# Kernel optimization log

Hardware: AMD Instinct MI355X
Metric: run time of the kernel (lower is better)

## Reference

```python
import jax, jax.numpy as jnp
import numpy as np

B, C, QK, T, S = 16, 256, 32, 15, 31


def _conv1x1(x, w, b):
    # 1x1 conv as channel matmul; w: [out, in]
    return jnp.einsum("oc,bchw->bohw", w, x) + b[None, :, None, None]


def _spatial_attn(x, qw, qb, kw, kb, vw, vb, g):
    Bn, Cn, H, W = x.shape
    N = H * W
    q = _conv1x1(x, qw, qb).reshape(Bn, -1, N)  # [B,QK,N]
    k = _conv1x1(x, kw, kb).reshape(Bn, -1, N)  # [B,QK,N]
    v = _conv1x1(x, vw, vb).reshape(Bn, Cn, N)  # [B,C,N]
    energy = jnp.einsum("bqn,bqm->bnm", q, k)   # [B,N,N]
    A = jax.nn.softmax(energy, axis=-1)
    out = g * jnp.einsum("bcm,bnm->bcn", v, A)
    return out.reshape(Bn, Cn, H, W)


def _channel_attn_calc(x):
    Bn, Cn = x.shape[0], x.shape[1]
    f = x.reshape(Bn, Cn, -1)
    e = jnp.einsum("bcn,bdn->bcd", f, f)  # [B,C,C]
    e = jnp.max(e, axis=-1, keepdims=True) - e
    return jax.nn.softmax(e, axis=-1)


def _channel_attn_use(x, A, w):
    Bn, Cn = x.shape[0], x.shape[1]
    v = x.reshape(Bn, Cn, -1)
    return (w * jnp.einsum("bcd,bdn->bcn", A, v)).reshape(x.shape)


def _mod_deform_conv(x, ow, ob, w, b):
    # Modulated deformable conv (DCNv2) 3x3, pad 1, stride 1.
    Bn, Cn, H, W = x.shape
    om = jax.lax.conv_general_dilated(x, ow, (1, 1), ((1, 1), (1, 1)),
                                      dimension_numbers=("NCHW", "OIHW", "NCHW"))
    om = om + ob[None, :, None, None]  # [B,27,H,W]
    off_y, off_x, mask = om[:, :9], om[:, 9:18], jax.nn.sigmoid(om[:, 18:])
    ky, kx = jnp.meshgrid(jnp.arange(3), jnp.arange(3), indexing="ij")
    py = off_y + jnp.arange(H)[None, None, :, None] + (ky.reshape(9) - 1)[None, :, None, None]
    px = off_x + jnp.arange(W)[None, None, None, :] + (kx.reshape(9) - 1)[None, :, None, None]
    y0f = jnp.floor(py); x0f = jnp.floor(px)
    wy = py - y0f; wx = px - x0f
    y0 = y0f.astype(jnp.int32); x0 = x0f.astype(jnp.int32)
    xf = x.reshape(Bn, Cn, H * W)

    def gather(yi, xi, wgt):
        valid = (yi >= 0) & (yi < H) & (xi >= 0) & (xi < W)
        idx = (jnp.clip(yi, 0, H - 1) * W + jnp.clip(xi, 0, W - 1)).reshape(Bn, -1)
        g = jax.vmap(lambda a, i: a[:, i])(xf, idx).reshape(Bn, Cn, 9, H, W)
        return g * (wgt * valid.astype(x.dtype))[:, None]

    val = (gather(y0, x0, (1 - wy) * (1 - wx)) + gather(y0, x0 + 1, (1 - wy) * wx)
           + gather(y0 + 1, x0, wy * (1 - wx)) + gather(y0 + 1, x0 + 1, wy * wx))
    val = val * mask[:, None]  # [B,C,9,H,W]
    return jnp.einsum("bckhw,ock->bohw", val, w.reshape(w.shape[0], Cn, 9)) + b[None, :, None, None]


def _forward(template_features, sr_features,
             t_sp_qw, t_sp_qb, t_sp_kw, t_sp_kb, t_sp_vw, t_sp_vb, t_sp_g,
             s_sp_qw, s_sp_qb, s_sp_kw, s_sp_kb, s_sp_vw, s_sp_vb, s_sp_g,
             w_t_ch, w_s_ch, w_s2t, w_t2s,
             t_off_w, t_off_b, t_dcn_w, t_dcn_b,
             s_off_w, s_off_b, s_dcn_w, s_dcn_b):
    t, s = template_features, sr_features
    t_sp = _spatial_attn(t, t_sp_qw, t_sp_qb, t_sp_kw, t_sp_kb, t_sp_vw, t_sp_vb, t_sp_g)
    s_sp = _spatial_attn(s, s_sp_qw, s_sp_qb, s_sp_kw, s_sp_kb, s_sp_vw, s_sp_vb, s_sp_g)
    tA = _channel_attn_calc(t)
    sA = _channel_attn_calc(s)
    t_ch = _channel_attn_use(t, tA, w_t_ch)
    s_ch = _channel_attn_use(s, sA, w_s_ch)
    t_x = _channel_attn_use(t, sA, w_s2t)   # sr->template cross attention
    s_x = _channel_attn_use(s, tA, w_t2s)   # template->sr cross attention
    t_out = t + t_sp + t_ch + t_x
    s_out = s + s_sp + s_ch + s_x
    t_out = _mod_deform_conv(t_out, t_off_w, t_off_b, t_dcn_w, t_dcn_b)
    s_out = _mod_deform_conv(s_out, s_off_w, s_off_b, s_dcn_w, s_dcn_b)
    return t_out, s_out


def setup_inputs() -> dict:
    key = jax.random.key(0)
    ks = jax.random.split(key, 28)
    r = lambda i, shape, sc=0.05: jax.random.normal(ks[i], shape, dtype=jnp.float32) * sc
    return {
        "template_features": jax.random.normal(ks[0], (B, C, T, T), dtype=jnp.float32),
        "sr_features": jax.random.normal(ks[1], (B, C, S, S), dtype=jnp.float32),
        "t_sp_qw": r(2, (QK, C)), "t_sp_qb": r(3, (QK,)),
        "t_sp_kw": r(4, (QK, C)), "t_sp_kb": r(5, (QK,)),
        "t_sp_vw": r(6, (C, C)), "t_sp_vb": r(7, (C,)), "t_sp_g": r(8, (1,), 0.5),
        "s_sp_qw": r(9, (QK, C)), "s_sp_qb": r(10, (QK,)),
        "s_sp_kw": r(11, (QK, C)), "s_sp_kb": r(12, (QK,)),
        "s_sp_vw": r(13, (C, C)), "s_sp_vb": r(14, (C,)), "s_sp_g": r(15, (1,), 0.5),
        "w_t_ch": r(16, (1,), 0.5), "w_s_ch": r(17, (1,), 0.5),
        "w_s2t": r(18, (1,), 0.5), "w_t2s": r(19, (1,), 0.5),
        "t_off_w": r(20, (27, C, 3, 3), 0.01), "t_off_b": r(21, (27,), 0.01),
        "t_dcn_w": r(22, (C, C, 3, 3)), "t_dcn_b": r(23, (C,)),
        "s_off_w": r(24, (27, C, 3, 3), 0.01), "s_off_b": r(25, (27,), 0.01),
        "s_dcn_w": r(26, (C, C, 3, 3)), "s_dcn_b": r(27, (C,)),
    }


def reference(template_features, sr_features,
              t_sp_qw, t_sp_qb, t_sp_kw, t_sp_kb, t_sp_vw, t_sp_vb, t_sp_g,
              s_sp_qw, s_sp_qb, s_sp_kw, s_sp_kb, s_sp_vw, s_sp_vb, s_sp_g,
              w_t_ch, w_s_ch, w_s2t, w_t2s,
              t_off_w, t_off_b, t_dcn_w, t_dcn_b,
              s_off_w, s_off_b, s_dcn_w, s_dcn_b):
    return _forward(template_features, sr_features,
                    t_sp_qw, t_sp_qb, t_sp_kw, t_sp_kb, t_sp_vw, t_sp_vb, t_sp_g,
                    s_sp_qw, s_sp_qb, s_sp_kw, s_sp_kb, s_sp_vw, s_sp_vb, s_sp_g,
                    w_t_ch, w_s_ch, w_s2t, w_t2s,
                    t_off_w, t_off_b, t_dcn_w, t_dcn_b,
                    s_off_w, s_off_b, s_dcn_w, s_dcn_b)
```

## Files before the change

kernel.cpp:

```cpp
#include <hip/hip_runtime.h>
#include <hip/hip_bf16.h>
#include <cmath>

typedef __attribute__((ext_vector_type(8))) short bf16x8;
typedef __attribute__((ext_vector_type(4))) float f32x4;

__device__ inline ushort f2bf(float f) {
  __hip_bfloat16 h = __float2bfloat16(f);
  return *reinterpret_cast<ushort*>(&h);
}
__device__ inline float bf2f(ushort u) {
  return __uint_as_float((uint)u << 16);
}
__device__ inline float bflo(uint x) { return __uint_as_float(x << 16); }
__device__ inline float bfhi(uint x) { return __uint_as_float(x & 0xffff0000u); }

__device__ inline bool fdecode(int totalS, int gxS, int gyS, int gxT, int gyT,
                               int& bx, int& by, int& bz, bool& isT) {
  const int total = gridDim.x;
  const int id = blockIdx.x;
  int wid = (id & 7) * (total >> 3) + (id >> 3);
  const int totalT = gxT * gyT * 16;
  if (wid >= totalS + totalT) return false;
  isT = wid >= totalS;
  int lid = isT ? wid - totalS : wid;
  const int gx = isT ? gxT : gxS;
  const int gy = isT ? gyT : gyS;
  bx = lid % gx;
  lid /= gx;
  by = lid % gy;
  bz = lid / gy;
  return true;
}

__global__ __launch_bounds__(256) void prep_weights_kernel(
    const float* __restrict__ t_qw, const float* __restrict__ t_qb,
    const float* __restrict__ t_kw, const float* __restrict__ t_kb,
    const float* __restrict__ s_qw, const float* __restrict__ s_qb,
    const float* __restrict__ s_kw, const float* __restrict__ s_kb,
    const float* __restrict__ t_vw, const float* __restrict__ t_vb,
    const float* __restrict__ s_vw, const float* __restrict__ s_vb,
    const float* __restrict__ t_off_w, const float* __restrict__ s_off_w,
    const float* __restrict__ t_dcn_w, const float* __restrict__ s_dcn_w,
    ushort* __restrict__ Wall_t, ushort* __restrict__ Wall_s,
    float* __restrict__ biasAll_t, float* __restrict__ biasAll_s,
    ushort* __restrict__ owb_t, ushort* __restrict__ owb_s,
    ushort* __restrict__ Awb_t, ushort* __restrict__ Awb_s) {
  int i = blockIdx.x * 256 + threadIdx.x;
  if (i < 81920) {
    const int r = i >> 8, c = i & 255;
    float v;
    if (r < 256) v = t_vw[(size_t)r * 256 + c];
    else if (r < 288) v = t_qw[(size_t)(r - 256) * 256 + c];
    else v = t_kw[(size_t)(r - 288) * 256 + c];
    Wall_t[i] = f2bf(v);
    return;
  }
  i -= 81920;
  if (i < 81920) {
    const int r = i >> 8, c = i & 255;
    float v;
    if (r < 256) v = s_vw[(size_t)r * 256 + c];
    else if (r < 288) v = s_qw[(size_t)(r - 256) * 256 + c];
    else v = s_kw[(size_t)(r - 288) * 256 + c];
    Wall_s[i] = f2bf(v);
    return;
  }
  i -= 81920;
  if (i < 320) {
    biasAll_t[i] = (i < 256) ? t_vb[i] : ((i < 288) ? t_qb[i - 256] : t_kb[i - 288]);
    return;
  }
  i -= 320;
  if (i < 320) {
    biasAll_s[i] = (i < 256) ? s_vb[i] : ((i < 288) ? s_qb[i - 256] : s_kb[i - 288]);
    return;
  }
  i -= 320;
  if (i < 73728) {
    const int o = i / 2304, k = i % 2304, tap = k >> 8, c = k & 255;
    owb_t[i] = (o < 27) ? f2bf(t_off_w[(size_t)o * 2304 + c * 9 + tap]) : (ushort)0;
    return;
  }
  i -= 73728;
  if (i < 73728) {
    const int o = i / 2304, k = i % 2304, tap = k >> 8, c = k & 255;
    owb_s[i] = (o < 27) ? f2bf(s_off_w[(size_t)o * 2304 + c * 9 + tap]) : (ushort)0;
    return;
  }
  i -= 73728;
  if (i < 589824) {
    const int frag = i >> 9, within = i & 511;
    const int lane = within >> 3, j = within & 7;
    const int mt = frag / 72, kt = frag % 72;
    const int o = mt * 16 + (lane & 15);
    const int k = kt * 32 + (lane >> 4) * 8 + j;
    const int tap = k >> 8, c = k & 255;
    Awb_t[i] = f2bf(t_dcn_w[(size_t)o * 2304 + c * 9 + tap]);
    return;
  }
  i -= 589824;
  if (i < 589824) {
    const int frag = i >> 9, within = i & 511;
    const int lane = within >> 3, j = within & 7;
    const int mt = frag / 72, kt = frag % 72;
    const int o = mt * 16 + (lane & 15);
    const int k = kt * 32 + (lane >> 4) * 8 + j;
    const int tap = k >> 8, c = k & 255;
    Awb_s[i] = f2bf(s_dcn_w[(size_t)o * 2304 + c * 9 + tap]);
  }
}

__global__ __launch_bounds__(256) void cast_transpose_fused_kernel(
    const float* __restrict__ xS, ushort* __restrict__ oS, ushort* __restrict__ pS,
    int NS_, int NRS_, int NpS_,
    const float* __restrict__ xT, ushort* __restrict__ oT, ushort* __restrict__ pT,
    int NT_, int NRT_, int NpT_) {
  constexpr int C = 256;
  __shared__ float T[64][65];
  int bx, by, bz; bool isT;
  if (!fdecode(1024, 16, 4, 4, 4, bx, by, bz, isT)) return;
  const float* x = isT ? xT : xS;
  ushort* xTo = isT ? oT : oS;
  ushort* xbf = isT ? pT : pS;
  const int N = isT ? NT_ : NS_;
  const int NR = isT ? NRT_ : NRS_;
  const int Np = isT ? NpT_ : NpS_;
  const int b = bz;
  const int n0 = bx * 64, c0 = by * 64;
  const float* xb = x + (size_t)b * C * N;
  const int tid = threadIdx.x;
  for (int u = tid; u < 4096; u += 256) {
    const int cc = u >> 6, nn = u & 63;
    const int gn = n0 + nn;
    T[cc][nn] = (gn < N) ? xb[(size_t)(c0 + cc) * N + gn] : 0.f;
  }
  __syncthreads();
  ushort* ob = xTo + (size_t)b * NR * C;
  for (int u = tid; u < 4096; u += 256) {
    const int nn = u >> 6, cc = u & 63;
    ob[(size_t)(n0 + nn) * C + c0 + cc] = f2bf(T[cc][nn]);
  }
  ushort* pb = xbf + (size_t)b * C * Np;
  for (int u = tid; u < 4096; u += 256) {
    const int cc = u >> 6, nn = u & 63;
    const int gn = n0 + nn;
    if (gn < Np) pb[(size_t)(c0 + cc) * Np + gn] = f2bf(T[cc][nn]);
  }
}

__global__ __launch_bounds__(256) void proj_fused_kernel(
    const ushort* __restrict__ WallS, const float* __restrict__ bS,
    const ushort* __restrict__ BtS, ushort* __restrict__ vS,
    float* __restrict__ qkS, int NS_, int NpS_, int NRS_,
    const ushort* __restrict__ WallT, const float* __restrict__ bT,
    const ushort* __restrict__ BtT, ushort* __restrict__ vT,
    float* __restrict__ qkT, int NT_, int NpT_, int NRT_) {
  constexpr int C = 256;
  __shared__ ushort Asm[64][40];
  __shared__ ushort Bsm[64][40];
  int bx, by, bz; bool isT;
  if (!fdecode(1280, 16, 5, 4, 5, bx, by, bz, isT)) return;
  const ushort* Wall = isT ? WallT : WallS;
  const float* bias = isT ? bT : bS;
  const ushort* Bt = isT ? BtT : BtS;
  ushort* vbf = isT ? vT : vS;
  float* qk = isT ? qkT : qkS;
  const int N = isT ? NT_ : NS_, Np = isT ? NpT_ : NpS_, NR = isT ? NRT_ : NRS_;
  const int n0 = bx * 64, m0 = by * 64, b = bz;
  const ushort* Ab = Wall + (size_t)m0 * C;
  const ushort* Bb = Bt + (size_t)b * NR * C;
  const int tid = threadIdx.x, lane = tid & 63, w = tid >> 6;
  f32x4 acc[4];
#pragma unroll
  for (int i = 0; i < 4; i++) acc[i] = (f32x4){0.f, 0.f, 0.f, 0.f};
  for (int k0 = 0; k0 < C; k0 += 32) {
    {
      const int row = tid >> 2, seg = tid & 3;
      *reinterpret_cast<uint4*>(&Asm[row][seg * 8]) =
          *reinterpret_cast<const uint4*>(&Ab[(size_t)row * C + k0 + seg * 8]);
    }
    {
      const int row = tid >> 2, seg = tid & 3;
      *reinterpret_cast<uint4*>(&Bsm[row][seg * 8]) =
          *reinterpret_cast<const uint4*>(&Bb[(size_t)(n0 + row) * C + k0 + seg * 8]);
    }
    __syncthreads();
    const int koff = (lane >> 4) * 8;
    const bf16x8 bfr = *reinterpret_cast<const bf16x8*>(&Bsm[w * 16 + (lane & 15)][koff]);
#pragma unroll
    for (int mf = 0; mf < 4; mf++) {
      const bf16x8 af = *reinterpret_cast<const bf16x8*>(&Asm[mf * 16 + (lane & 15)][koff]);
      acc[mf] = __builtin_amdgcn_mfma_f32_16x16x32_bf16(af, bfr, acc[mf], 0, 0, 0);
    }
    __syncthreads();
  }
  const int gn = n0 + w * 16 + (lane & 15);
#pragma unroll
  for (int mf = 0; mf < 4; mf++) {
    const int mbase = m0 + mf * 16 + ((lane >> 4) * 4);
#pragma unroll
    for (int rr = 0; rr < 4; rr++) {
      const int m = mbase + rr;
      if (m < 256) {
        if (gn < Np) {
          ushort v = (gn < N) ? f2bf(acc[mf][rr] + bias[m]) : (ushort)0;
          vbf[((size_t)b * 256 + m) * Np + gn] = v;
        }
      } else {
        if (gn < N)
          qk[((size_t)b * 64 + (m - 256)) * N + gn] = acc[mf][rr] + bias[m];
      }
    }
  }
}

__global__ __launch_bounds__(256) void softmax_mcomb_kernel(
    const float* __restrict__ Atc, const float* __restrict__ Asc,
    const float* __restrict__ w_t_ch, const float* __restrict__ w_s2t,
    const float* __restrict__ w_s_ch, const float* __restrict__ w_t2s,
    ushort* __restrict__ Mc_t, ushort* __restrict__ Mc_s) {
  const int row = blockIdx.x;
  const int tid = threadIdx.x;
  __shared__ float red[8];
  const size_t idx = (size_t)row * 256 + tid;
  const float a = -Atc[idx];
  const float s = -Asc[idx];
  float ma = a, ms = s;
#pragma unroll
  for (int off = 32; off; off >>= 1) {
    ma = fmaxf(ma, __shfl_xor(ma, off, 64));
    ms = fmaxf(ms, __shfl_xor(ms, off, 64));
  }
  if ((tid & 63) == 0) { red[tid >> 6] = ma; red[4 + (tid >> 6)] = ms; }
  __syncthreads();
  if (tid == 0) {
    float m1 = red[0], m2 = red[4];
    for (int i = 1; i < 4; i++) { m1 = fmaxf(m1, red[i]); m2 = fmaxf(m2, red[4 + i]); }
    red[0] = m1; red[4] = m2;
  }
  __syncthreads();
  ma = red[0]; ms = red[4];
  __syncthreads();
  const float ea = __expf(a - ma), es = __expf(s - ms);
  float sa = ea, ss = es;
#pragma unroll
  for (int off = 32; off; off >>= 1) {
    sa += __shfl_xor(sa, off, 64);
    ss += __shfl_xor(ss, off, 64);
  }
  if ((tid & 63) == 0) { red[tid >> 6] = sa; red[4 + (tid >> 6)] = ss; }
  __syncthreads();
  if (tid == 0) {
    float t1 = 0.f, t2 = 0.f;
    for (int i = 0; i < 4; i++) { t1 += red[i]; t2 += red[4 + i]; }
    red[0] = t1; red[4] = t2;
  }
  __syncthreads();
  const float Pa = ea / red[0], Ps = es / red[4];
  Mc_t[idx] = f2bf(w_t_ch[0] * Pa + w_s2t[0] * Ps);
  Mc_s[idx] = f2bf(w_s_ch[0] * Ps + w_t2s[0] * Pa);
}

template <int EPI>
__global__ __launch_bounds__(256) void gemm_fused_kernel(
    const ushort* __restrict__ AS, int aPerB_S, const ushort* __restrict__ BtS,
    const float* __restrict__ biasS, ushort* __restrict__ outBfS,
    float* __restrict__ outFS, int NS_, int NpS_, int NRS_, int KpS_,
    const ushort* __restrict__ AT, int aPerB_T, const ushort* __restrict__ BtT,
    const float* __restrict__ biasT, ushort* __restrict__ outBfT,
    float* __restrict__ outFT, int NT_, int NpT_, int NRT_, int KpT_,
    int totalS, int gxS, int gxT) {
  constexpr int CM = 256, BM = 128, NW = 4, NF = 2, WN = 2;
  __shared__ ushort Asm[BM][40];
  __shared__ ushort Bsm[64][40];
  int bx, by, bz; bool isT;
  if (!fdecode(totalS, gxS, 2, gxT, 2, bx, by, bz, isT)) return;
  const ushort* A = isT ? AT : AS;
  const ushort* Bt = isT ? BtT : BtS;
  const float* bias = isT ? biasT : biasS;
  ushort* outBf = isT ? outBfT : outBfS;
  float* outF = isT ? outFT : outFS;
  const int aPerBatch = isT ? aPerB_T : aPerB_S;
  const int N = isT ? NT_ : NS_, Np = isT ? NpT_ : NpS_;
  const int NR = isT ? NRT_ : NRS_, Kp = isT ? KpT_ : KpS_;
  const int n0 = bx * 64, m0 = by * BM, b = bz;
  const ushort* Ab = A + (size_t)(aPerBatch ? b : 0) * CM * Kp;
  const ushort* Bb = Bt + (size_t)b * NR * Kp;
  const int tid = threadIdx.x, lane = tid & 63, w = tid >> 6;
  const int wr = w / WN, wc = w % WN;
  f32x4 acc[4][NF];
#pragma unroll
  for (int i = 0; i < 4; i++)
#pragma unroll
    for (int j = 0; j < NF; j++) acc[i][j] = (f32x4){0.f, 0.f, 0.f, 0.f};
  for (int k0 = 0; k0 < Kp; k0 += 32) {
    for (int u = tid; u < BM * 4; u += NW * 64) {
      const int row = u >> 2, seg = u & 3;
      *reinterpret_cast<uint4*>(&Asm[row][seg * 8]) =
          *reinterpret_cast<const uint4*>(&Ab[(size_t)(m0 + row) * Kp + k0 + seg * 8]);
    }
    for (int u = tid; u < 64 * 4; u += NW * 64) {
      const int row = u >> 2, seg = u & 3;
      *reinterpret_cast<uint4*>(&Bsm[row][seg * 8]) =
          *reinterpret_cast<const uint4*>(&Bb[(size_t)(n0 + row) * Kp + k0 + seg * 8]);
    }
    __syncthreads();
    const int koff = (lane >> 4) * 8;
    bf16x8 af[4], bfr[NF];
#pragma unroll
    for (int mf = 0; mf < 4; mf++)
      af[mf] = *reinterpret_cast<const bf16x8*>(&Asm[wr * 64 + mf * 16 + (lane & 15)][koff]);
#pragma unroll
    for (int nf = 0; nf < NF; nf++)
      bfr[nf] = *reinterpret_cast<const bf16x8*>(&Bsm[wc * NF * 16 + nf * 16 + (lane & 15)][koff]);
#pragma unroll
    for (int mf = 0; mf < 4; mf++)
#pragma unroll
      for (int nf = 0; nf < NF; nf++)
        acc[mf][nf] = __builtin_amdgcn_mfma_f32_16x16x32_bf16(af[mf], bfr[nf], acc[mf][nf], 0, 0, 0);
    __syncthreads();
  }
#pragma unroll
  for (int mf = 0; mf < 4; mf++) {
    const int mbase = m0 + wr * 64 + mf * 16 + ((lane >> 4) * 4);
#pragma unroll
    for (int nf = 0; nf < NF; nf++) {
      const int gn = n0 + wc * NF * 16 + nf * 16 + (lane & 15);
      if (EPI == 0) {
#pragma unroll
        for (int rr = 0; rr < 4; rr++) {
          const int m = mbase + rr;
          if (gn < Np) {
            ushort v = (gn < N) ? f2bf(acc[mf][nf][rr] + bias[m]) : (ushort)0;
            outBf[((size_t)b * CM + m) * Np + gn] = v;
          }
        }
      } else {
#pragma unroll
        for (int rr = 0; rr < 4; rr++) {
          if (gn < N)
            outF[((size_t)b * CM + mbase + rr) * N + gn] = acc[mf][nf][rr];
        }
      }
    }
  }
  (void)NR;
}

__global__ __launch_bounds__(256) void energy_fused_kernel(
    const float* __restrict__ qkS, ushort* __restrict__ SS, int NS_, int NpS_,
    const float* __restrict__ qkT, ushort* __restrict__ ST, int NT_, int NpT_) {
  __shared__ ushort Aq[64][40];
  __shared__ ushort Bk[64][40];
  int bx, by, bz; bool isT;
  if (!fdecode(4096, 16, 16, 4, 4, bx, by, bz, isT)) return;
  const float* qk = isT ? qkT : qkS;
  ushort* Sbf = isT ? ST : SS;
  const int N = isT ? NT_ : NS_, Np = isT ? NpT_ : NpS_;
  const int m0 = bx * 64, n0 = by * 64, b = bz;
  const float* qb = qk + (size_t)b * 64 * N;
  const float* kb = qb + (size_t)32 * N;
  const int tid = threadIdx.x, lane = tid & 63, w = tid >> 6;
  for (int u = tid; u < 2048; u += 256) {
    const int c = u >> 6, nn = u & 63;
    const int gn = n0 + nn, gm = m0 + nn;
    Aq[nn][c] = (gn < N) ? f2bf(qb[(size_t)c * N + gn]) : (ushort)0;
    Bk[nn][c] = (gm < N) ? f2bf(kb[(size_t)c * N + gm]) : (ushort)0;
  }
  __syncthreads();
  const int koff = (lane >> 4) * 8;
  const bf16x8 af = *reinterpret_cast<const bf16x8*>(&Aq[w * 16 + (lane & 15)][koff]);
  f32x4 acc[4];
#pragma unroll
  for (int j = 0; j < 4; j++) {
    const bf16x8 bf = *reinterpret_cast<const bf16x8*>(&Bk[j * 16 + (lane & 15)][koff]);
    acc[j] = __builtin_amdgcn_mfma_f32_16x16x32_bf16(af, bf, (f32x4){0.f, 0.f, 0.f, 0.f}, 0, 0, 0);
  }
#pragma unroll
  for (int j = 0; j < 4; j++) {
    const int m = m0 + j * 16 + (lane & 15);
    if (m >= Np) continue;
#pragma unroll
    for (int r = 0; r < 4; r++) {
      const int n = n0 + w * 16 + (lane >> 4) * 4 + r;
      if (n < N) Sbf[((size_t)b * N + n) * Np + m] = (m < N) ? f2bf(acc[j][r]) : (ushort)0;
    }
  }
}

__global__ __launch_bounds__(256) void softmax_bf16_fused_kernel(
    ushort* __restrict__ Ss, int Ns, int Nps, ushort* __restrict__ St, int Nt,
    int Npt, int rowsS) {
  __shared__ float buf[992];
  __shared__ float red[4];
  const int row = blockIdx.x;
  ushort* r;
  int N;
  if (row < rowsS) {
    r = Ss + (size_t)row * Nps;
    N = Ns;
  } else {
    r = St + (size_t)(row - rowsS) * Npt;
    N = Nt;
  }
  const int tid = threadIdx.x;
  float mx = -1e30f;
  for (int i = tid; i < N; i += 256) {
    float f = bf2f(r[i]);
    buf[i] = f;
    mx = fmaxf(mx, f);
  }
#pragma unroll
  for (int off = 32; off; off >>= 1) mx = fmaxf(mx, __shfl_xor(mx, off, 64));
  if ((tid & 63) == 0) red[tid >> 6] = mx;
  __syncthreads();
  if (tid == 0) {
    float m2 = red[0];
    for (int i = 1; i < 4; i++) m2 = fmaxf(m2, red[i]);
    red[0] = m2;
  }
  __syncthreads();
  mx = red[0];
  __syncthreads();
  float s = 0.f;
  for (int i = tid; i < N; i += 256) {
    float v = __expf(buf[i] - mx);
    buf[i] = v;
    s += v;
  }
#pragma unroll
  for (int off = 32; off; off >>= 1) s += __shfl_xor(s, off, 64);
  if ((tid & 63) == 0) red[tid >> 6] = s;
  __syncthreads();
  if (tid == 0) {
    float t = 0.f;
    for (int i = 0; i < 4; i++) t += red[i];
    red[0] = t;
  }
  __syncthreads();
  const float inv = 1.f / red[0];
  for (int i = tid; i < N; i += 256) r[i] = f2bf(buf[i] * inv);
}

__global__ __launch_bounds__(256) void pv_chan_fused_kernel(
    const ushort* __restrict__ vS, const ushort* __restrict__ SS,
    const ushort* __restrict__ McS, const ushort* __restrict__ xTS,
    const float* __restrict__ xS, const float* __restrict__ gS,
    ushort* __restrict__ xsTS, int NS_, int NpS_, int NRS_,
    const ushort* __restrict__ vT, const ushort* __restrict__ ST,
    const ushort* __restrict__ McT, const ushort* __restrict__ xTT,
    const float* __restrict__ xT_, const float* __restrict__ gT,
    ushort* __restrict__ xsTT, int NT_, int NpT_, int NRT_) {
  constexpr int C = 256, BM = 128, NW = 4, NF = 2, WN = 2;
  __shared__ ushort Asm[BM][40];
  __shared__ ushort Bsm[64][40];
  int bx, by, bz; bool isT;
  if (!fdecode(512, 16, 2, 4, 2, bx, by, bz, isT)) return;
  const ushort* vbf = isT ? vT : vS;
  const ushort* Sbf = isT ? ST : SS;
  const ushort* Mc = isT ? McT : McS;
  const ushort* xTb = isT ? xTT : xTS;
  const float* x = isT ? xT_ : xS;
  const float* gp = isT ? gT : gS;
  ushort* xsT = isT ? xsTT : xsTS;
  const int N = isT ? NT_ : NS_, Np = isT ? NpT_ : NpS_;
  const int NR = isT ? NRT_ : NRS_;
  const int n0 = bx * 64, m0 = by * BM, b = bz;
  const int tid = threadIdx.x, lane = tid & 63, w = tid >> 6;
  const int wr = w / WN, wc = w % WN;
// ... 330 lines not shown
#pragma unroll
      for (int rr = 0; rr < 4; rr++)
        out[((size_t)b * C + mbase + rr) * N + gn] = acc[mf][rr] + bias[mbase + rr];
    }
  }
}

extern "C" void kernel_launch(void* const* d_in, const int* in_sizes, int n_in,
                              void* d_out, int out_size, void* d_ws, size_t ws_size,
                              hipStream_t stream) {
  const float* t_in = (const float*)d_in[0];
  const float* s_in = (const float*)d_in[1];
  const float* t_qw = (const float*)d_in[2];
  const float* t_qb = (const float*)d_in[3];
  const float* t_kw = (const float*)d_in[4];
  const float* t_kb = (const float*)d_in[5];
  const float* t_vw = (const float*)d_in[6];
  const float* t_vb = (const float*)d_in[7];
  const float* t_g = (const float*)d_in[8];
  const float* s_qw = (const float*)d_in[9];
  const float* s_qb = (const float*)d_in[10];
  const float* s_kw = (const float*)d_in[11];
  const float* s_kb = (const float*)d_in[12];
  const float* s_vw = (const float*)d_in[13];
  const float* s_vb = (const float*)d_in[14];
  const float* s_g = (const float*)d_in[15];
  const float* w_t_ch = (const float*)d_in[16];
  const float* w_s_ch = (const float*)d_in[17];
  const float* w_s2t = (const float*)d_in[18];
  const float* w_t2s = (const float*)d_in[19];
  const float* t_off_w = (const float*)d_in[20];
  const float* t_off_b = (const float*)d_in[21];
  const float* t_dcn_w = (const float*)d_in[22];
  const float* t_dcn_b = (const float*)d_in[23];
  const float* s_off_w = (const float*)d_in[24];
  const float* s_off_b = (const float*)d_in[25];
  const float* s_dcn_w = (const float*)d_in[26];
  const float* s_dcn_b = (const float*)d_in[27];
  (void)in_sizes; (void)n_in; (void)out_size; (void)ws_size;

  constexpr int Bn = 16, C = 256;
  constexpr int HT = 15, WT = 15, NT = HT * WT;
  constexpr int HS = 31, WS2 = 31, NS = HS * WS2;
  constexpr int NpT = 256, NpS = 992;
  constexpr int NRT = 256, NRS = 1024;

  float* ws = (float*)d_ws;
  size_t off = 0;
  auto alloc = [&](size_t n) {
    n = (n + 3) & ~(size_t)3;
    float* p = ws + off; off += n; return p;
  };
  auto allocU = [&](size_t nu) { return (ushort*)alloc((nu + 1) / 2); };

  float* qk_t = alloc((size_t)Bn * 64 * NT);
  float* qk_s = alloc((size_t)Bn * 64 * NS);
  ushort* Wall_t = allocU((size_t)320 * C);
  ushort* Wall_s = allocU((size_t)320 * C);
  float* biasAll_t = alloc(320);
  float* biasAll_s = alloc(320);
  ushort* xT_t = allocU((size_t)Bn * NRT * C);
  ushort* xT_s = allocU((size_t)Bn * NRS * C);
  ushort* xbf_t = allocU((size_t)Bn * C * NpT);
  ushort* xbf_s = allocU((size_t)Bn * C * NpS);
  ushort* v_tbf = allocU((size_t)Bn * C * NpT);
  ushort* v_sbf = allocU((size_t)Bn * C * NpS);
  ushort* S_t = allocU((size_t)Bn * NT * NpT);
  ushort* S_s = allocU((size_t)Bn * NS * NpS);
  ushort* xsT_t = allocU((size_t)Bn * NRT * C);
  ushort* xsT_s = allocU((size_t)Bn * NRS * C);
  float* Atc = alloc((size_t)Bn * C * C);
  float* Asc = alloc((size_t)Bn * C * C);
  ushort* Mc_t = allocU((size_t)Bn * C * C);
  ushort* Mc_s = allocU((size_t)Bn * C * C);
  ushort* owb_t = allocU((size_t)32 * 2304);
  ushort* owb_s = allocU((size_t)32 * 2304);
  ushort* Awb_t = allocU((size_t)256 * 2304);
  ushort* Awb_s = allocU((size_t)256 * 2304);
  uint4* prep_t = (uint4*)alloc((size_t)Bn * 9 * NT * 4);
  uint4* prep_s = (uint4*)alloc((size_t)Bn * 9 * NS * 4);

  dim3 blk(256);

  prep_weights_kernel<<<dim3((1491584 + 255) / 256), blk, 0, stream>>>(
      t_qw, t_qb, t_kw, t_kb, s_qw, s_qb, s_kw, s_kb,
      t_vw, t_vb, s_vw, s_vb, t_off_w, s_off_w, t_dcn_w, s_dcn_w,
      Wall_t, Wall_s, biasAll_t, biasAll_s, owb_t, owb_s, Awb_t, Awb_s);

  cast_transpose_fused_kernel<<<dim3(1280), blk, 0, stream>>>(
      s_in, xT_s, xbf_s, NS, NRS, NpS, t_in, xT_t, xbf_t, NT, NRT, NpT);

  proj_fused_kernel<<<dim3(1600), blk, 0, stream>>>(
      Wall_s, biasAll_s, xT_s, v_sbf, qk_s, NS, NpS, NRS,
      Wall_t, biasAll_t, xT_t, v_tbf, qk_t, NT, NpT, NRT);

  energy_fused_kernel<<<dim3(4352), blk, 0, stream>>>(
      qk_s, S_s, NS, NpS, qk_t, S_t, NT, NpT);

  softmax_bf16_fused_kernel<<<dim3(Bn * NS + Bn * NT), blk, 0, stream>>>(
      S_s, NS, NpS, S_t, NT, NpT, Bn * NS);

  gemm_fused_kernel<2><<<dim3(256), blk, 0, stream>>>(
      xbf_s, 1, xbf_s, nullptr, nullptr, Asc, C, C, C, NpS,
      xbf_t, 1, xbf_t, nullptr, nullptr, Atc, C, C, C, NpT,
      128, 4, 4);

  softmax_mcomb_kernel<<<dim3(Bn * C), blk, 0, stream>>>(
      Atc, Asc, w_t_ch, w_s2t, w_s_ch, w_t2s, Mc_t, Mc_s);

  pv_chan_fused_kernel<<<dim3(640), blk, 0, stream>>>(
      v_sbf, S_s, Mc_s, xT_s, s_in, s_g, xsT_s, NS, NpS, NRS,
      v_tbf, S_t, Mc_t, xT_t, t_in, t_g, xsT_t, NT, NpT, NRT);

  offconv_prep_fused_kernel<<<dim3(320), blk, 0, stream>>>(
      xsT_s, owb_s, s_off_b, prep_s, HS, WS2, NS, NRS,
      xsT_t, owb_t, t_off_b, prep_t, HT, WT, NT, NRT);

  float* out_t = (float*)d_out;
  float* out_s = out_t + (size_t)Bn * C * NT;
  dcn_fused_kernel<<<dim3(640), dim3(512), 0, stream>>>(
      xsT_s, prep_s, Awb_s, s_dcn_b, out_s, NS, WS2, NRS,
      xsT_t, prep_t, Awb_t, t_dcn_b, out_t, NT, WT, NRT);
}
```

Before: 290.0 us.

## Merge independent launches: prep+cast, projection+gram, energy+channel softmax

Combines independent kernels into single launches by partitioning the grid into virtual block ranges: weight prep with cast/transpose, the q/k/v projection with the channel Gram GEMM, and the spatial energy with the channel softmax/combination. This cuts the launch count from nine to six, removing launch gaps and letting independent work fill the GPU together. In exchange, shared memory is sized for the larger branch (Asm grows to 128 rows in the projection path), which may lower occupancy. The gram branch writes with stride C instead of N, which matches the C×C output.

```diff
diff --git a/kernel.cpp b/kernel.cpp
--- a/kernel.cpp
+++ b/kernel.cpp
@@ -33,7 +33,21 @@
   return true;
 }
 
-__global__ __launch_bounds__(256) void prep_weights_kernel(
+__device__ inline void vdecode(int v, int vtotal, int totalS, int gxS, int gyS,
+                               int gxT, int gyT, int& bx, int& by, int& bz,
+                               bool& isT) {
+  int wid = (v & 7) * (vtotal >> 3) + (v >> 3);
+  isT = wid >= totalS;
+  int lid = isT ? wid - totalS : wid;
+  const int gx = isT ? gxT : gxS;
+  const int gy = isT ? gyT : gyS;
+  bx = lid % gx;
+  lid /= gx;
+  by = lid % gy;
+  bz = lid / gy;
+}
+
+__global__ __launch_bounds__(256) void prep_cast_fused_kernel(
     const float* __restrict__ t_qw, const float* __restrict__ t_qb,
     const float* __restrict__ t_kw, const float* __restrict__ t_kb,
     const float* __restrict__ s_qw, const float* __restrict__ s_qb,
@@ -45,81 +59,83 @@
     ushort* __restrict__ Wall_t, ushort* __restrict__ Wall_s,
     float* __restrict__ biasAll_t, float* __restrict__ biasAll_s,
     ushort* __restrict__ owb_t, ushort* __restrict__ owb_s,
-    ushort* __restrict__ Awb_t, ushort* __restrict__ Awb_s) {
-  int i = blockIdx.x * 256 + threadIdx.x;
-  if (i < 81920) {
-    const int r = i >> 8, c = i & 255;
-    float v;
-    if (r < 256) v = t_vw[(size_t)r * 256 + c];
-    else if (r < 288) v = t_qw[(size_t)(r - 256) * 256 + c];
-    else v = t_kw[(size_t)(r - 288) * 256 + c];
-    Wall_t[i] = f2bf(v);
+    ushort* __restrict__ Awb_t, ushort* __restrict__ Awb_s,
+    const float* __restrict__ xS, ushort* __restrict__ oS,
+    ushort* __restrict__ pS, int NS_, int NRS_, int NpS_,
+    const float* __restrict__ xT, ushort* __restrict__ oT,
+    ushort* __restrict__ pT, int NT_, int NRT_, int NpT_) {
+  __shared__ float T[64][65];
+  const int tid = threadIdx.x;
+  const int vid = blockIdx.x;
+  if (vid < 5832) {
+    int i = vid * 256 + tid;
+    if (i < 81920) {
+      const int r = i >> 8, c = i & 255;
+      float v;
+      if (r < 256) v = t_vw[(size_t)r * 256 + c];
+      else if (r < 288) v = t_qw[(size_t)(r - 256) * 256 + c];
+      else v = t_kw[(size_t)(r - 288) * 256 + c];
+      Wall_t[i] = f2bf(v);
+      return;
+    }
+    i -= 81920;
+    if (i < 81920) {
+      const int r = i >> 8, c = i & 255;
+      float v;
+      if (r < 256) v = s_vw[(size_t)r * 256 + c];
+      else if (r < 288) v = s_qw[(size_t)(r - 256) * 256 + c];
+      else v = s_kw[(size_t)(r - 288) * 256 + c];
+      Wall_s[i] = f2bf(v);
+      return;
+    }
+    i -= 81920;
+    if (i < 320) {
+      biasAll_t[i] = (i < 256) ? t_vb[i] : ((i < 288) ? t_qb[i - 256] : t_kb[i - 288]);
+      return;
+    }
+    i -= 320;
+    if (i < 320) {
+      biasAll_s[i] = (i < 256) ? s_vb[i] : ((i < 288) ? s_qb[i - 256] : s_kb[i - 288]);
+      return;
+    }
+    i -= 320;
+    if (i < 73728) {
+      const int o = i / 2304, k = i % 2304, tap = k >> 8, c = k & 255;
+      owb_t[i] = (o < 27) ? f2bf(t_off_w[(size_t)o * 2304 + c * 9 + tap]) : (ushort)0;
+      return;
+    }
+    i -= 73728;
+    if (i < 73728) {
+      const int o = i / 2304, k = i % 2304, tap = k >> 8, c = k & 255;
+      owb_s[i] = (o < 27) ? f2bf(s_off_w[(size_t)o * 2304 + c * 9 + tap]) : (ushort)0;
+      return;
+    }
+    i -= 73728;
+    if (i < 589824) {
+      const int frag = i >> 9, within = i & 511;
+      const int lane = within >> 3, j = within & 7;
+      const int mt = frag / 72, kt = frag % 72;
+      const int o = mt * 16 + (lane & 15);
+      const int k = kt * 32 + (lane >> 4) * 8 + j;
+      const int tap = k >> 8, c = k & 255;
+      Awb_t[i] = f2bf(t_dcn_w[(size_t)o * 2304 + c * 9 + tap]);
+      return;
+    }
+    i -= 589824;
+    if (i < 589824) {
+      const int frag = i >> 9, within = i & 511;
+      const int lane = within >> 3, j = within & 7;
+      const int mt = frag / 72, kt = frag % 72;
+      const int o = mt * 16 + (lane & 15);
+      const int k = kt * 32 + (lane >> 4) * 8 + j;
+      const int tap = k >> 8, c = k & 255;
+      Awb_s[i] = f2bf(s_dcn_w[(size_t)o * 2304 + c * 9 + tap]);
+    }
     return;
   }
-  i -= 81920;
-  if (i < 81920) {
-    const int r = i >> 8, c = i & 255;
-    float v;
-    if (r < 256) v = s_vw[(size_t)r * 256 + c];
-    else if (r < 288) v = s_qw[(size_t)(r - 256) * 256 + c];
-    else v = s_kw[(size_t)(r - 288) * 256 + c];
-    Wall_s[i] = f2bf(v);
-    return;
-  }
-  i -= 81920;
-  if (i < 320) {
-    biasAll_t[i] = (i < 256) ? t_vb[i] : ((i < 288) ? t_qb[i - 256] : t_kb[i - 288]);
-    return;
-  }
-  i -= 320;
-  if (i < 320) {
-    biasAll_s[i] = (i < 256) ? s_vb[i] : ((i < 288) ? s_qb[i - 256] : s_kb[i - 288]);
-    return;
-  }
-  i -= 320;
-  if (i < 73728) {
-    const int o = i / 2304, k = i % 2304, tap = k >> 8, c = k & 255;
-    owb_t[i] = (o < 27) ? f2bf(t_off_w[(size_t)o * 2304 + c * 9 + tap]) : (ushort)0;
-    return;
-  }
-  i -= 73728;
-  if (i < 73728) {
-    const int o = i / 2304, k = i % 2304, tap = k >> 8, c = k & 255;
-    owb_s[i] = (o < 27) ? f2bf(s_off_w[(size_t)o * 2304 + c * 9 + tap]) : (ushort)0;
-    return;
-  }
-  i -= 73728;
-  if (i < 589824) {
-    const int frag = i >> 9, within = i & 511;
-    const int lane = within >> 3, j = within & 7;
-    const int mt = frag / 72, kt = frag % 72;
-    const int o = mt * 16 + (lane & 15);
-    const int k = kt * 32 + (lane >> 4) * 8 + j;
-    const int tap = k >> 8, c = k & 255;
-    Awb_t[i] = f2bf(t_dcn_w[(size_t)o * 2304 + c * 9 + tap]);
-    return;
-  }
-  i -= 589824;
-  if (i < 589824) {
-    const int frag = i >> 9, within = i & 511;
-    const int lane = within >> 3, j = within & 7;
-    const int mt = frag / 72, kt = frag % 72;
-    const int o = mt * 16 + (lane & 15);
-    const int k = kt * 32 + (lane >> 4) * 8 + j;
-    const int tap = k >> 8, c = k & 255;
-    Awb_s[i] = f2bf(s_dcn_w[(size_t)o * 2304 + c * 9 + tap]);
-  }
-}
-
-__global__ __launch_bounds__(256) void cast_transpose_fused_kernel(
-    const float* __restrict__ xS, ushort* __restrict__ oS, ushort* __restrict__ pS,
-    int NS_, int NRS_, int NpS_,
-    const float* __restrict__ xT, ushort* __restrict__ oT, ushort* __restrict__ pT,
-    int NT_, int NRT_, int NpT_) {
   constexpr int C = 256;
-  __shared__ float T[64][65];
   int bx, by, bz; bool isT;
-  if (!fdecode(1024, 16, 4, 4, 4, bx, by, bz, isT)) return;
+  vdecode(vid - 5832, 1280, 1024, 16, 4, 4, 4, bx, by, bz, isT);
   const float* x = isT ? xT : xS;
   ushort* xTo = isT ? oT : oS;
   ushort* xbf = isT ? pT : pS;
@@ -129,7 +145,6 @@
   const int b = bz;
   const int n0 = bx * 64, c0 = by * 64;
   const float* xb = x + (size_t)b * C * N;
-  const int tid = threadIdx.x;
   for (int u = tid; u < 4096; u += 256) {
     const int cc = u >> 6, nn = u & 63;
     const int gn = n0 + nn;
@@ -149,243 +164,217 @@
   }
 }
 
-__global__ __launch_bounds__(256) void proj_fused_kernel(
+__global__ __launch_bounds__(256) void proj_gram_fused_kernel(
     const ushort* __restrict__ WallS, const float* __restrict__ bS,
     const ushort* __restrict__ BtS, ushort* __restrict__ vS,
     float* __restrict__ qkS, int NS_, int NpS_, int NRS_,
     const ushort* __restrict__ WallT, const float* __restrict__ bT,
     const ushort* __restrict__ BtT, ushort* __restrict__ vT,
-    float* __restrict__ qkT, int NT_, int NpT_, int NRT_) {
+    float* __restrict__ qkT, int NT_, int NpT_, int NRT_,
+    const ushort* __restrict__ xbfS, float* __restrict__ AscP, int KpS_,
+    const ushort* __restrict__ xbfT, float* __restrict__ AtcP, int KpT_) {
   constexpr int C = 256;
-  __shared__ ushort Asm[64][40];
+  __shared__ ushort Asm[128][40];
   __shared__ ushort Bsm[64][40];
-  int bx, by, bz; bool isT;
-  if (!fdecode(1280, 16, 5, 4, 5, bx, by, bz, isT)) return;
-  const ushort* Wall = isT ? WallT : WallS;
-  const float* bias = isT ? bT : bS;
-  const ushort* Bt = isT ? BtT : BtS;
-  ushort* vbf = isT ? vT : vS;
-  float* qk = isT ? qkT : qkS;
-  const int N = isT ? NT_ : NS_, Np = isT ? NpT_ : NpS_, NR = isT ? NRT_ : NRS_;
-  const int n0 = bx * 64, m0 = by * 64, b = bz;
-  const ushort* Ab = Wall + (size_t)m0 * C;
-  const ushort* Bb = Bt + (size_t)b * NR * C;
   const int tid = threadIdx.x, lane = tid & 63, w = tid >> 6;
-  f32x4 acc[4];
-#pragma unroll
-  for (int i = 0; i < 4; i++) acc[i] = (f32x4){0.f, 0.f, 0.f, 0.f};
-  for (int k0 = 0; k0 < C; k0 += 32) {
-    {
-      const int row = tid >> 2, seg = tid & 3;
-      *reinterpret_cast<uint4*>(&Asm[row][seg * 8]) =
-          *reinterpret_cast<const uint4*>(&Ab[(size_t)row * C + k0 + seg * 8]);
-    }
-    {
-      const int row = tid >> 2, seg = tid & 3;
-      *reinterpret_cast<uint4*>(&Bsm[row][seg * 8]) =
-          *reinterpret_cast<const uint4*>(&Bb[(size_t)(n0 + row) * C + k0 + seg * 8]);
-    }
-    __syncthreads();
-    const int koff = (lane >> 4) * 8;
-    const bf16x8 bfr = *reinterpret_cast<const bf16x8*>(&Bsm[w * 16 + (lane & 15)][koff]);
+  const int vid = blockIdx.x;
+  if (vid < 1600) {
+    int bx, by, bz; bool isT;
+    vdecode(vid, 1600, 1280, 16, 5, 4, 5, bx, by, bz, isT);
+    const ushort* Wall = isT ? WallT : WallS;
+    const float* bias = isT ? bT : bS;
+    const ushort* Bt = isT ? BtT : BtS;
+    ushort* vbf = isT ? vT : vS;
+    float* qk = isT ? qkT : qkS;
+    const int N = isT ? NT_ : NS_, Np = isT ? NpT_ : NpS_, NR = isT ? NRT_ : NRS_;
+    const int n0 = bx * 64, m0 = by * 64, b = bz;
+    const ushort* Ab = Wall + (size_t)m0 * C;
+    const ushort* Bb = Bt + (size_t)b * NR * C;
+    f32x4 acc[4];
+#pragma unroll
+    for (int i = 0; i < 4; i++) acc[i] = (f32x4){0.f, 0.f, 0.f, 0.f};
+    for (int k0 = 0; k0 < C; k0 += 32) {
+      {
+        const int row = tid >> 2, seg = tid & 3;
+        *reinterpret_cast<uint4*>(&Asm[row][seg * 8]) =
+            *reinterpret_cast<const uint4*>(&Ab[(size_t)row * C + k0 + seg * 8]);
+        *reinterpret_cast<uint4*>(&Bsm[row][seg * 8]) =
+            *reinterpret_cast<const uint4*>(&Bb[(size_t)(n0 + row) * C + k0 + seg * 8]);
+      }
+      __syncthreads();
+      const int koff = (lane >> 4) * 8;
+      const bf16x8 bfr = *reinterpret_cast<const bf16x8*>(&Bsm[w * 16 + (lane & 15)][koff]);
+#pragma unroll
+      for (int mf = 0; mf < 4; mf++) {
+        const bf16x8 af = *reinterpret_cast<const bf16x8*>(&Asm[mf * 16 + (lane & 15)][koff]);
+        acc[mf] = __builtin_amdgcn_mfma_f32_16x16x32_bf16(af, bfr, acc[mf], 0, 0, 0);
+      }
+      __syncthreads();
+    }
+    const int gn = n0 + w * 16 + (lane & 15);
 #pragma unroll
     for (int mf = 0; mf < 4; mf++) {
-      const bf16x8 af = *reinterpret_cast<const bf16x8*>(&Asm[mf * 16 + (lane & 15)][koff]);
-      acc[mf] = __builtin_amdgcn_mfma_f32_16x16x32_bf16(af, bfr, acc[mf], 0, 0, 0);
-    }
-    __syncthreads();
-  }
-  const int gn = n0 + w * 16 + (lane & 15);
-#pragma unroll
-  for (int mf = 0; mf < 4; mf++) {
-    const int mbase = m0 + mf * 16 + ((lane >> 4) * 4);
-#pragma unroll
-    for (int rr = 0; rr < 4; rr++) {
-      const int m = mbase + rr;
-      if (m < 256) {
-        if (gn < Np) {
-          ushort v = (gn < N) ? f2bf(acc[mf][rr] + bias[m]) : (ushort)0;
-          vbf[((size_t)b * 256 + m) * Np + gn] = v;
+      const int mbase = m0 + mf * 16 + ((lane >> 4) * 4);
+#pragma unroll
+      for (int rr = 0; rr < 4; rr++) {
+        const int m = mbase + rr;
+        if (m < 256) {
+          if (gn < Np) {
+            ushort v = (gn < N) ? f2bf(acc[mf][rr] + bias[m]) : (ushort)0;
+            vbf[((size_t)b * 256 + m) * Np + gn] = v;
+          }
+        } else {
+          if (gn < N)
+            qk[((size_t)b * 64 + (m - 256)) * N + gn] = acc[mf][rr] + bias[m];
         }
-      } else {
-        if (gn < N)
-          qk[((size_t)b * 64 + (m - 256)) * N + gn] = acc[mf][rr] + bias[m];
-      }
-    }
-  }
-}
-
-__global__ __launch_bounds__(256) void softmax_mcomb_kernel(
+      }
+    }
+    return;
+  }
+  {
+    constexpr int BM = 128, NW = 4, NF = 2, WN = 2;
+    int bx, by, bz; bool isT;
+    vdecode(vid - 1600, 256, 128, 4, 2, 4, 2, bx, by, bz, isT);
+    const ushort* A = isT ? xbfT : xbfS;
+    float* outF = isT ? AtcP : AscP;
+    const int Kp = isT ? KpT_ : KpS_;
+    const int n0 = bx * 64, m0 = by * BM, b = bz;
+    const ushort* Ab = A + (size_t)b * C * Kp;
+    const int wr = w / WN, wc = w % WN;
+    f32x4 acc[4][NF];
+#pragma unroll
+    for (int i = 0; i < 4; i++)
+#pragma unroll
+      for (int j = 0; j < NF; j++) acc[i][j] = (f32x4){0.f, 0.f, 0.f, 0.f};
+    for (int k0 = 0; k0 < Kp; k0 += 32) {
+      for (int u = tid; u < BM * 4; u += NW * 64) {
+        const int row = u >> 2, seg = u & 3;
+        *reinterpret_cast<uint4*>(&Asm[row][seg * 8]) =
+            *reinterpret_cast<const uint4*>(&Ab[(size_t)(m0 + row) * Kp + k0 + seg * 8]);
+      }
+      for (int u = tid; u < 64 * 4; u += NW * 64) {
+        const int row = u >> 2, seg = u & 3;
+        *reinterpret_cast<uint4*>(&Bsm[row][seg * 8]) =
+            *reinterpret_cast<const uint4*>(&Ab[(size_t)(n0 + row) * Kp + k0 + seg * 8]);
+      }
+      __syncthreads();
+      const int koff = (lane >> 4) * 8;
+      bf16x8 af[4], bfr[NF];
+#pragma unroll
+      for (int mf = 0; mf < 4; mf++)
+        af[mf] = *reinterpret_cast<const bf16x8*>(&Asm[wr * 64 + mf * 16 + (lane & 15)][koff]);
+#pragma unroll
+      for (int nf = 0; nf < NF; nf++)
+        bfr[nf] = *reinterpret_cast<const bf16x8*>(&Bsm[wc * NF * 16 + nf * 16 + (lane & 15)][koff]);
+#pragma unroll
+      for (int mf = 0; mf < 4; mf++)
+#pragma unroll
+        for (int nf = 0; nf < NF; nf++)
+          acc[mf][nf] = __builtin_amdgcn_mfma_f32_16x16x32_bf16(af[mf], bfr[nf], acc[mf][nf], 0, 0, 0);
+      __syncthreads();
+    }
+#pragma unroll
+    for (int mf = 0; mf < 4; mf++) {
+      const int mbase = m0 + wr * 64 + mf * 16 + ((lane >> 4) * 4);
+#pragma unroll
+      for (int nf = 0; nf < NF; nf++) {
+        const int gn = n0 + wc * NF * 16 + nf * 16 + (lane & 15);
+#pragma unroll
+        for (int rr = 0; rr < 4; rr++)
+          outF[((size_t)b * C + mbase + rr) * C + gn] = acc[mf][nf][rr];
+      }
+    }
+  }
+}
+
+__global__ __launch_bounds__(256) void energy_mcomb_fused_kernel(
+    const float* __restrict__ qkS, ushort* __restrict__ SS, int NS_, int NpS_,
+    const float* __restrict__ qkT, ushort* __restrict__ ST, int NT_, int NpT_,
     const float* __restrict__ Atc, const float* __restrict__ Asc,
     const float* __restrict__ w_t_ch, const float* __restrict__ w_s2t,
     const float* __restrict__ w_s_ch, const float* __restrict__ w_t2s,
     ushort* __restrict__ Mc_t, ushort* __restrict__ Mc_s) {
-  const int row = blockIdx.x;
+  __shared__ ushort Aq[64][40];
+  __shared__ ushort Bk[64][40];
+  __shared__ float red[8];
   const int tid = threadIdx.x;
-  __shared__ float red[8];
-  const size_t idx = (size_t)row * 256 + tid;
-  const float a = -Atc[idx];
-  const float s = -Asc[idx];
-  float ma = a, ms = s;
-#pragma unroll
-  for (int off = 32; off; off >>= 1) {
-    ma = fmaxf(ma, __shfl_xor(ma, off, 64));
-    ms = fmaxf(ms, __shfl_xor(ms, off, 64));
-  }
-  if ((tid & 63) == 0) { red[tid >> 6] = ma; red[4 + (tid >> 6)] = ms; }
-  __syncthreads();
-  if (tid == 0) {
-    float m1 = red[0], m2 = red[4];
-    for (int i = 1; i < 4; i++) { m1 = fmaxf(m1, red[i]); m2 = fmaxf(m2, red[4 + i]); }
-    red[0] = m1; red[4] = m2;
-  }
-  __syncthreads();
-  ma = red[0]; ms = red[4];
-  __syncthreads();
-  const float ea = __expf(a - ma), es = __expf(s - ms);
-  float sa = ea, ss = es;
-#pragma unroll
-  for (int off = 32; off; off >>= 1) {
-    sa += __shfl_xor(sa, off, 64);
-    ss += __shfl_xor(ss, off, 64);
-  }
-  if ((tid & 63) == 0) { red[tid >> 6] = sa; red[4 + (tid >> 6)] = ss; }
-  __syncthreads();
-  if (tid == 0) {
-    float t1 = 0.f, t2 = 0.f;
-    for (int i = 0; i < 4; i++) { t1 += red[i]; t2 += red[4 + i]; }
-    red[0] = t1; red[4] = t2;
-  }
-  __syncthreads();
-  const float Pa = ea / red[0], Ps = es / red[4];
-  Mc_t[idx] = f2bf(w_t_ch[0] * Pa + w_s2t[0] * Ps);
-  Mc_s[idx] = f2bf(w_s_ch[0] * Ps + w_t2s[0] * Pa);
-}
-
-template <int EPI>
-__global__ __launch_bounds__(256) void gemm_fused_kernel(
-    const ushort* __restrict__ AS, int aPerB_S, const ushort* __restrict__ BtS,
-    const float* __restrict__ biasS, ushort* __restrict__ outBfS,
-    float* __restrict__ outFS, int NS_, int NpS_, int NRS_, int KpS_,
-    const ushort* __restrict__ AT, int aPerB_T, const ushort* __restrict__ BtT,
-    const float* __restrict__ biasT, ushort* __restrict__ outBfT,
-    float* __restrict__ outFT, int NT_, int NpT_, int NRT_, int KpT_,
-    int totalS, int gxS, int gxT) {
-  constexpr int CM = 256, BM = 128, NW = 4, NF = 2, WN = 2;
-  __shared__ ushort Asm[BM][40];
-  __shared__ ushort Bsm[64][40];
-  int bx, by, bz; bool isT;
-  if (!fdecode(totalS, gxS, 2, gxT, 2, bx, by, bz, isT)) return;
-  const ushort* A = isT ? AT : AS;
-  const ushort* Bt = isT ? BtT : BtS;
-  const float* bias = isT ? biasT : biasS;
-  ushort* outBf = isT ? outBfT : outBfS;
-  float* outF = isT ? outFT : outFS;
-  const int aPerBatch = isT ? aPerB_T : aPerB_S;
-  const int N = isT ? NT_ : NS_, Np = isT ? NpT_ : NpS_;
-  const int NR = isT ? NRT_ : NRS_, Kp = isT ? KpT_ : KpS_;
-  const int n0 = bx * 64, m0 = by * BM, b = bz;
-  const ushort* Ab = A + (size_t)(aPerBatch ? b : 0) * CM * Kp;
-  const ushort* Bb = Bt + (size_t)b * NR * Kp;
-  const int tid = threadIdx.x, lane = tid & 63, w = tid >> 6;
-  const int wr = w / WN, wc = w % WN;
-  f32x4 acc[4][NF];
-#pragma unroll
-  for (int i = 0; i < 4; i++)
-#pragma unroll
-    for (int j = 0; j < NF; j++) acc[i][j] = (f32x4){0.f, 0.f, 0.f, 0.f};
-  for (int k0 = 0; k0 < Kp; k0 += 32) {
-    for (int u = tid; u < BM * 4; u += NW * 64) {
-      const int row = u >> 2, seg = u & 3;
-      *reinterpret_cast<uint4*>(&Asm[row][seg * 8]) =
-          *reinterpret_cast<const uint4*>(&Ab[(size_t)(m0 + row) * Kp + k0 + seg * 8]);
-    }
-    for (int u = tid; u < 64 * 4; u += NW * 64) {
-      const int row = u >> 2, seg = u & 3;
-      *reinterpret_cast<uint4*>(&Bsm[row][seg * 8]) =
-          *reinterpret_cast<const uint4*>(&Bb[(size_t)(n0 + row) * Kp + k0 + seg * 8]);
+  const int vid = blockIdx.x;
+  if (vid < 4352) {
+    int bx, by, bz; bool isT;
+    vdecode(vid, 4352, 4096, 16, 16, 4, 4, bx, by, bz, isT);
+    const float* qk = isT ? qkT : qkS;
+    ushort* Sbf = isT ? ST : SS;
+    const int N = isT ? NT_ : NS_, Np = isT ? NpT_ : NpS_;
+    const int m0 = bx * 64, n0 = by * 64, b = bz;
+    const float* qb = qk + (size_t)b * 64 * N;
+    const float* kb = qb + (size_t)32 * N;
+    const int lane = tid & 63, w = tid >> 6;
+    for (int u = tid; u < 2048; u += 256) {
+      const int c = u >> 6, nn = u & 63;
+      const int gn = n0 + nn, gm = m0 + nn;
+      Aq[nn][c] = (gn < N) ? f2bf(qb[(size_t)c * N + gn]) : (ushort)0;
+      Bk[nn][c] = (gm < N) ? f2bf(kb[(size_t)c * N + gm]) : (ushort)0;
     }
     __syncthreads();
     const int koff = (lane >> 4) * 8;
-    bf16x8 af[4], bfr[NF];
-#pragma unroll
-    for (int mf = 0; mf < 4; mf++)
-      af[mf] = *reinterpret_cast<const bf16x8*>(&Asm[wr * 64 + mf * 16 + (lane & 15)][koff]);
-#pragma unroll
-    for (int nf = 0; nf < NF; nf++)
-      bfr[nf] = *reinterpret_cast<const bf16x8*>(&Bsm[wc * NF * 16 + nf * 16 + (lane & 15)][koff]);
-#pragma unroll
-    for (int mf = 0; mf < 4; mf++)
-#pragma unroll
-      for (int nf = 0; nf < NF; nf++)
-        acc[mf][nf] = __builtin_amdgcn_mfma_f32_16x16x32_bf16(af[mf], bfr[nf], acc[mf][nf], 0, 0, 0);
+    const bf16x8 af = *reinterpret_cast<const bf16x8*>(&Aq[w * 16 + (lane & 15)][koff]);
+    f32x4 acc[4];
+#pragma unroll
+    for (int j = 0; j < 4; j++) {
+      const bf16x8 bf = *reinterpret_cast<const bf16x8*>(&Bk[j * 16 + (lane & 15)][koff]);
+      acc[j] = __builtin_amdgcn_mfma_f32_16x16x32_bf16(af, bf, (f32x4){0.f, 0.f, 0.f, 0.f}, 0, 0, 0);
+    }
+#pragma unroll
+    for (int j = 0; j < 4; j++) {
+      const int m = m0 + j * 16 + (lane & 15);
+      if (m >= Np) continue;
+#pragma unroll
+      for (int r = 0; r < 4; r++) {
+        const int n = n0 + w * 16 + (lane >> 4) * 4 + r;
+        if (n < N) Sbf[((size_t)b * N + n) * Np + m] = (m < N) ? f2bf(acc[j][r]) : (ushort)0;
+      }
+    }
+    return;
+  }
+  {
+    const int row = vid - 4352;
+    const size_t idx = (size_t)row * 256 + tid;
+    const float a = -Atc[idx];
+    const float s = -Asc[idx];
+    float ma = a, ms = s;
+#pragma unroll
+    for (int off = 32; off; off >>= 1) {
+      ma = fmaxf(ma, __shfl_xor(ma, off, 64));
+      ms = fmaxf(ms, __shfl_xor(ms, off, 64));
+    }
+    if ((tid & 63) == 0) { red[tid >> 6] = ma; red[4 + (tid >> 6)] = ms; }
     __syncthreads();
-  }
-#pragma unroll
-  for (int mf = 0; mf < 4; mf++) {
-    const int mbase = m0 + wr * 64 + mf * 16 + ((lane >> 4) * 4);
-#pragma unroll
-    for (int nf = 0; nf < NF; nf++) {
-      const int gn = n0 + wc * NF * 16 + nf * 16 + (lane & 15);
-      if (EPI == 0) {
-#pragma unroll
-        for (int rr = 0; rr < 4; rr++) {
-          const int m = mbase + rr;
-          if (gn < Np) {
-            ushort v = (gn < N) ? f2bf(acc[mf][nf][rr] + bias[m]) : (ushort)0;
-            outBf[((size_t)b * CM + m) * Np + gn] = v;
-          }
-        }
-      } else {
-#pragma unroll
-        for (int rr = 0; rr < 4; rr++) {
-          if (gn < N)
-            outF[((size_t)b * CM + mbase + rr) * N + gn] = acc[mf][nf][rr];
-        }
-      }
-    }
-  }
-  (void)NR;
-}
-
-__global__ __launch_bounds__(256) void energy_fused_kernel(
-    const float* __restrict__ qkS, ushort* __restrict__ SS, int NS_, int NpS_,
-    const float* __restrict__ qkT, ushort* __restrict__ ST, int NT_, int NpT_) {
-  __shared__ ushort Aq[64][40];
-  __shared__ ushort Bk[64][40];
-  int bx, by, bz; bool isT;
-  if (!fdecode(4096, 16, 16, 4, 4, bx, by, bz, isT)) return;
-  const float* qk = isT ? qkT : qkS;
-  ushort* Sbf = isT ? ST : SS;
-  const int N = isT ? NT_ : NS_, Np = isT ? NpT_ : NpS_;
-  const int m0 = bx * 64, n0 = by * 64, b = bz;
-  const float* qb = qk + (size_t)b * 64 * N;
-  const float* kb = qb + (size_t)32 * N;
-  const int tid = threadIdx.x, lane = tid & 63, w = tid >> 6;
-  for (int u = tid; u < 2048; u += 256) {
-    const int c = u >> 6, nn = u & 63;
-    const int gn = n0 + nn, gm = m0 + nn;
-    Aq[nn][c] = (gn < N) ? f2bf(qb[(size_t)c * N + gn]) : (ushort)0;
-    Bk[nn][c] = (gm < N) ? f2bf(kb[(size_t)c * N + gm]) : (ushort)0;
-  }
-  __syncthreads();
-  const int koff = (lane >> 4) * 8;
-  const bf16x8 af = *reinterpret_cast<const bf16x8*>(&Aq[w * 16 + (lane & 15)][koff]);
-  f32x4 acc[4];
-#pragma unroll
-  for (int j = 0; j < 4; j++) {
-    const bf16x8 bf = *reinterpret_cast<const bf16x8*>(&Bk[j * 16 + (lane & 15)][koff]);
-    acc[j] = __builtin_amdgcn_mfma_f32_16x16x32_bf16(af, bf, (f32x4){0.f, 0.f, 0.f, 0.f}, 0, 0, 0);
-  }
-#pragma unroll
-  for (int j = 0; j < 4; j++) {
-    const int m = m0 + j * 16 + (lane & 15);
-    if (m >= Np) continue;
-#pragma unroll
-    for (int r = 0; r < 4; r++) {
-      const int n = n0 + w * 16 + (lane >> 4) * 4 + r;
-      if (n < N) Sbf[((size_t)b * N + n) * Np + m] = (m < N) ? f2bf(acc[j][r]) : (ushort)0;
-    }
+    if (tid == 0) {
+      float m1 = red[0], m2 = red[4];
+      for (int i = 1; i < 4; i++) { m1 = fmaxf(m1, red[i]); m2 = fmaxf(m2, red[4 + i]); }
+      red[0] = m1; red[4] = m2;
+    }
+    __syncthreads();
+    ma = red[0]; ms = red[4];
+    __syncthreads();
+    const float ea = __expf(a - ma), es = __expf(s - ms);
+    float sa = ea, ss = es;
+#pragma unroll
+    for (int off = 32; off; off >>= 1) {
+      sa += __shfl_xor(sa, off, 64);
+      ss += __shfl_xor(ss, off, 64);
+    }
+    if ((tid & 63) == 0) { red[tid >> 6] = sa; red[4 + (tid >> 6)] = ss; }
+    __syncthreads();
+    if (tid == 0) {
+      float t1 = 0.f, t2 = 0.f;
+      for (int i = 0; i < 4; i++) { t1 += red[i]; t2 += red[4 + i]; }
+      red[0] = t1; red[4] = t2;
+    }
+    __syncthreads();
+    const float Pa = ea / red[0], Ps = es / red[4];
+    Mc_t[idx] = f2bf(w_t_ch[0] * Pa + w_s2t[0] * Ps);
+    Mc_s[idx] = f2bf(w_s_ch[0] * Ps + w_t2s[0] * Pa);
   }
 }
 
@@ -882,31 +871,23 @@
 
   dim3 blk(256);
 
-  prep_weights_kernel<<<dim3((1491584 + 255) / 256), blk, 0, stream>>>(
+  prep_cast_fused_kernel<<<dim3(5832 + 1280), blk, 0, stream>>>(
       t_qw, t_qb, t_kw, t_kb, s_qw, s_qb, s_kw, s_kb,
       t_vw, t_vb, s_vw, s_vb, t_off_w, s_off_w, t_dcn_w, s_dcn_w,
-      Wall_t, Wall_s, biasAll_t, biasAll_s, owb_t, owb_s, Awb_t, Awb_s);
-
-  cast_transpose_fused_kernel<<<dim3(1280), blk, 0, stream>>>(
+      Wall_t, Wall_s, biasAll_t, biasAll_s, owb_t, owb_s, Awb_t, Awb_s,
       s_in, xT_s, xbf_s, NS, NRS, NpS, t_in, xT_t, xbf_t, NT, NRT, NpT);
 
-  proj_fused_kernel<<<dim3(1600), blk, 0, stream>>>(
+  proj_gram_fused_kernel<<<dim3(1600 + 256), blk, 0, stream>>>(
       Wall_s, biasAll_s, xT_s, v_sbf, qk_s, NS, NpS, NRS,
-      Wall_t, biasAll_t, xT_t, v_tbf, qk_t, NT, NpT, NRT);
-
-  energy_fused_kernel<<<dim3(4352), blk, 0, stream>>>(
-      qk_s, S_s, NS, NpS, qk_t, S_t, NT, NpT);
+      Wall_t, biasAll_t, xT_t, v_tbf, qk_t, NT, NpT, NRT,
+      xbf_s, Asc, NpS, xbf_t, Atc, NpT);
+
+  energy_mcomb_fused_kernel<<<dim3(4352 + 4096), blk, 0, stream>>>(
+      qk_s, S_s, NS, NpS, qk_t, S_t, NT, NpT,
+      Atc, Asc, w_t_ch, w_s2t, w_s_ch, w_t2s, Mc_t, Mc_s);
 
   softmax_bf16_fused_kernel<<<dim3(Bn * NS + Bn * NT), blk, 0, stream>>>(
       S_s, NS, NpS, S_t, NT, NpT, Bn * NS);
-
-  gemm_fused_kernel<2><<<dim3(256), blk, 0, stream>>>(
-      xbf_s, 1, xbf_s, nullptr, nullptr, Asc, C, C, C, NpS,
-      xbf_t, 1, xbf_t, nullptr, nullptr, Atc, C, C, C, NpT,
-      128, 4, 4);
-
-  softmax_mcomb_kernel<<<dim3(Bn * C), blk, 0, stream>>>(
-      Atc, Asc, w_t_ch, w_s2t, w_s_ch, w_t2s, Mc_t, Mc_s);
 
   pv_chan_fused_kernel<<<dim3(640), blk, 0, stream>>>(
       v_sbf, S_s, Mc_s, xT_s, s_in, s_g, xsT_s, NS, NpS, NRS,
```

After: 273.3 us. 1.06x faster.
